# Optimization experiments

Hardware: AMD Instinct MI355X
Metric: run time of the kernel (lower is better)

Reference implementation:

```python
import jax, jax.numpy as jnp
import numpy as np

N_NODES = 100000
N_REL = 8
N_EDGES = 1_600_000
ED = 64   # entity_dim
RD = 64   # relation_dim
H = 4     # attention heads
A = 16    # attention dim per head
D1, D2 = 32, 16  # conv_dim_list


def _leaky(x):
    return jax.nn.leaky_relu(x, 0.01)  # nn.LeakyReLU default slope


def _l2norm(x):
    n = jnp.sqrt(jnp.sum(x * x, axis=1, keepdims=True))
    return x / jnp.maximum(n, 1e-12)  # F.normalize(p=2, dim=1)


def setup_inputs() -> dict:
    key = jax.random.key(0)
    ks = jax.random.split(key, 16)
    s = 0.1
    return dict(
        src=jax.random.randint(ks[0], (N_EDGES,), 0, N_NODES),
        dst=jax.random.randint(ks[1], (N_EDGES,), 0, N_NODES),
        etype=jax.random.randint(ks[2], (N_EDGES,), 0, N_REL),
        node_ids=jnp.arange(N_NODES),
        user_ids=jax.random.randint(ks[3], (1000,), 0, N_NODES),
        item_ids=jax.random.randint(ks[4], (4096,), 0, N_NODES),
        entity_embed=jax.random.normal(ks[5], (N_NODES, ED)) * s,
        rel_embed=jax.random.normal(ks[6], (N_REL, RD)) * s,
        W_R=jax.random.normal(ks[7], (N_REL, ED, RD)) * s,
        W_A=jax.random.normal(ks[8], (RD, H, A)) * s,
        W1_0=jax.random.normal(ks[9], (ED, D1 // H)) * s,
        b1_0=jnp.zeros((D1 // H,)),
        W2_0=jax.random.normal(ks[10], (ED, D1 // H)) * s,
        b2_0=jnp.zeros((D1 // H,)),
        W1_1=jax.random.normal(ks[11], (D1, D2 // H)) * s,
        b1_1=jnp.zeros((D2 // H,)),
        W2_1=jax.random.normal(ks[12], (D1, D2 // H)) * s,
        b2_1=jnp.zeros((D2 // H,)),
    )


def _compute_attention(entity_embed, rel_embed, W_R, W_A, src, dst, etype):
    # relation-specific edge attention: tanh(e_src W_r W_A) * tanh(e_dst W_r W_A + r W_A)
    WA_flat = W_A.reshape(RD, H * A)
    W_ra = jnp.einsum('rij,jk->rik', W_R, WA_flat)          # [R, ED, H*A]
    proj = jnp.einsum('ne,rek->rnk', entity_embed, W_ra)    # [R, N, H*A]
    r_emb_a = rel_embed @ WA_flat                           # [R, H*A]
    r_mul_t = jnp.tanh(proj[etype, src])                    # [E, H*A]
    r_mul_h = jnp.tanh(proj[etype, dst] + r_emb_a[etype])   # [E, H*A]
    att = (r_mul_t * r_mul_h).reshape(-1, H, A).sum(-1)     # [E, H]
    # edge softmax over incoming edges of each dst node, per head
    m = jax.ops.segment_max(att, dst, num_segments=N_NODES)
    m = jnp.where(jnp.isfinite(m), m, 0.0)
    e = jnp.exp(att - m[dst])
    z = jax.ops.segment_sum(e, dst, num_segments=N_NODES)
    return e / jnp.maximum(z[dst], 1e-12)                   # [E, H]


def _bi_layer(ego, att, src, dst, W1, b1, W2, b2, out_dim):
    # u_mul_e + sum: message = node[src] (broadcast over heads) * att[:, :, None]
    in_dim = ego.shape[1]
    msg = ego[src][:, None, :] * att[:, :, None]            # [E, H, in]
    N_h = jax.ops.segment_sum(msg, dst, num_segments=N_NODES)  # [N, H, in]
    node = ego[:, None, :]                                  # [N, 1, in]
    out1 = _leaky((node + N_h).reshape(-1, in_dim) @ W1 + b1).reshape(N_NODES, out_dim)
    out2 = _leaky((node * N_h).reshape(-1, in_dim) @ W2 + b2).reshape(N_NODES, out_dim)
    return out1 + out2  # dropout p=0 (eval)


def reference(src, dst, etype, node_ids, user_ids, item_ids,
              entity_embed, rel_embed, W_R, W_A,
              W1_0, b1_0, W2_0, b2_0, W1_1, b1_1, W2_1, b2_1):
    att = _compute_attention(entity_embed, rel_embed, W_R, W_A, src, dst, etype)
    ego = entity_embed[node_ids]
    ego1 = _bi_layer(ego, att, src, dst, W1_0, b1_0, W2_0, b2_0, D1)
    ego2 = _bi_layer(ego1, att, src, dst, W1_1, b1_1, W2_1, b2_1, D2)
    all_embed = jnp.concatenate([ego, _l2norm(ego1), _l2norm(ego2)], axis=1)  # [N, 112]
    return all_embed[user_ids] @ all_embed[item_ids].T     # [1000, 4096]
```

## Files before the change

### kernel.cpp

```cpp
#include <hip/hip_runtime.h>
#include <hip/hip_bf16.h>
#include <math.h>

#define NN 100000
#define NR 8
#define NE 1600000

typedef __attribute__((ext_vector_type(8))) short short8v;
typedef __attribute__((ext_vector_type(4))) float float4v;
typedef __attribute__((ext_vector_type(2))) float float2v;

__device__ inline float bf2f(unsigned short u) {
  union { unsigned int i; float f; } v; v.i = ((unsigned int)u) << 16; return v.f;
}
__device__ inline unsigned short f2bf(float f) {
  __hip_bfloat16 h = __float2bfloat16(f);
  return *reinterpret_cast<unsigned short*>(&h);
}
__device__ inline float fast_tanh(float x) {
  float ex = __expf(2.f * x);
  return 1.f - 2.f * __builtin_amdgcn_rcpf(ex + 1.f);
}
__device__ inline unsigned char f2fp8(float f) {
  unsigned int p = __builtin_amdgcn_cvt_pk_fp8_f32(f, f, 0, false);
  return (unsigned char)(p & 0xff);
}

__global__ void k_prep(const float* __restrict__ W_R, const float* __restrict__ W_A,
                       const float* __restrict__ rel, unsigned short* __restrict__ Wbf,
                       float* __restrict__ r_emb_a) {
  int tid = blockIdx.x * 256 + threadIdx.x;
  if (tid < NR * 64 * 64) {
    int r = tid >> 12;
    int i = (tid >> 6) & 63;
    int k = tid & 63;
    float acc = 0.f;
    const float* wr = W_R + (r * 64 + i) * 64;
    for (int j = 0; j < 64; ++j) acc += wr[j] * W_A[j * 64 + k];
    Wbf[(r * 64 + k) * 64 + i] = f2bf(acc);
  } else if (tid < NR * 64 * 64 + NR * 64) {
    int idx = tid - NR * 64 * 64;
    int r = idx >> 6, k = idx & 63;
    float acc = 0.f;
    for (int j = 0; j < 64; ++j) acc += rel[r * 64 + j] * W_A[j * 64 + k];
    r_emb_a[idx] = acc;
  }
}

__global__ void k_cvt(const float* __restrict__ E, unsigned short* __restrict__ Ebf) {
  int i = blockIdx.x * 256 + threadIdx.x;
  float4 v = ((const float4*)E)[i];
  ushort4 o;
  o.x = f2bf(v.x); o.y = f2bf(v.y); o.z = f2bf(v.z); o.w = f2bf(v.w);
  ((ushort4*)Ebf)[i] = o;
}

__global__ void k_proj(const unsigned short* __restrict__ Ebf,
                       const unsigned short* __restrict__ Wbf,
                       const float* __restrict__ rea,
                       unsigned char* __restrict__ T1, unsigned char* __restrict__ T2) {
  int wv = threadIdx.x >> 6, lane = threadIdx.x & 63;
  int n0 = blockIdx.x * 64 + wv * 16;
  int mrow = lane & 15, kg = lane >> 4;
  int nodeA = n0 + mrow;
  if (nodeA >= NN) nodeA = NN - 1;
  const short8v a0 = *(const short8v*)(Ebf + (long)nodeA * 64 + kg * 8);
  const short8v a1 = *(const short8v*)(Ebf + (long)nodeA * 64 + 32 + kg * 8);
  int orow = kg * 4;
  for (int ct = 0; ct < 32; ++ct) {
    int c = ct * 16 + mrow;
    const short8v b0 = *(const short8v*)(Wbf + c * 64 + kg * 8);
    const short8v b1 = *(const short8v*)(Wbf + c * 64 + 32 + kg * 8);
    float4v acc = {0.f, 0.f, 0.f, 0.f};
    acc = __builtin_amdgcn_mfma_f32_16x16x32_bf16(a0, b0, acc, 0, 0, 0);
    acc = __builtin_amdgcn_mfma_f32_16x16x32_bf16(a1, b1, acc, 0, 0, 0);
    float rv = rea[c];
    int r = c >> 6, kk = c & 63;
#pragma unroll
    for (int i = 0; i < 4; ++i) {
      int nd = n0 + orow + i;
      if (nd < NN) {
        long base = ((long)r * NN + nd) * 64 + kk;
        T1[base] = f2fp8(fast_tanh(acc[i]));
        T2[base] = f2fp8(fast_tanh(acc[i] + rv));
      }
    }
  }
}

__global__ void k_hist(const int* __restrict__ dst, int* __restrict__ cnt) {
  int e = blockIdx.x * 256 + threadIdx.x;
  if (e < NE) atomicAdd(&cnt[dst[e]], 1);
}

#define SCAN_B 1024
#define NSCAN ((NN + SCAN_B - 1) / SCAN_B)

__global__ void k_scan1(const int* __restrict__ cnt, int* __restrict__ rowp,
                        int* __restrict__ bsum) {
  __shared__ int s[SCAN_B];
  int t = threadIdx.x, g = blockIdx.x * SCAN_B + t;
  s[t] = (g < NN) ? cnt[g] : 0;
  __syncthreads();
  for (int off = 1; off < SCAN_B; off <<= 1) {
    int x = (t >= off) ? s[t - off] : 0;
    __syncthreads();
    s[t] += x;
    __syncthreads();
  }
  if (g < NN) rowp[g + 1] = s[t];
  if (t == SCAN_B - 1) bsum[blockIdx.x] = s[t];
}

__global__ void k_scan2(int* bsum) {
  if (threadIdx.x == 0) {
    int acc = 0;
    for (int i = 0; i < NSCAN; ++i) { int v = bsum[i]; bsum[i] = acc; acc += v; }
  }
}

__global__ void k_scan3(int* rowp, const int* __restrict__ bsum) {
  int t = threadIdx.x, g = blockIdx.x * SCAN_B + t;
  if (g < NN) rowp[g + 1] += bsum[blockIdx.x];
  if (g == 0) rowp[0] = 0;
}

__global__ void k_scatter(const int* __restrict__ src, const int* __restrict__ dst,
                          const int* __restrict__ etype, const int* __restrict__ rowp,
                          int* __restrict__ cur, uint2* __restrict__ rec) {
  int e = blockIdx.x * 256 + threadIdx.x;
  if (e >= NE) return;
  int d = dst[e];
  int p = rowp[d] + atomicAdd(&cur[d], 1);
  uint2 rv;
  rv.x = ((unsigned int)src[e] << 3) | (unsigned int)etype[e];
  rv.y = (unsigned int)d;
  rec[p] = rv;
}

__global__ void k_att(const unsigned char* __restrict__ T1,
                      const unsigned char* __restrict__ T2,
                      const uint2* __restrict__ rec, int* __restrict__ srcs,
                      float* __restrict__ att) {
  int gid = blockIdx.x * 256 + threadIdx.x;
  int e = gid >> 2;
  int h = gid & 3;
  if (e >= NE) return;
  uint2 rv = rec[e];
  int r = rv.x & 7;
  int s = rv.x >> 3;
  int d = (int)rv.y;
  const uint4 av = *(const uint4*)(T1 + ((long)r * NN + s) * 64 + h * 16);
  const uint4 bv = *(const uint4*)(T2 + ((long)r * NN + d) * 64 + h * 16);
  const unsigned int* ap = (const unsigned int*)&av;
  const unsigned int* bp = (const unsigned int*)&bv;
  float acc = 0.f;
#pragma unroll
  for (int i = 0; i < 4; ++i) {
    float2v a0 = __builtin_amdgcn_cvt_pk_f32_fp8(ap[i], false);
    float2v a1 = __builtin_amdgcn_cvt_pk_f32_fp8(ap[i], true);
    float2v b0 = __builtin_amdgcn_cvt_pk_f32_fp8(bp[i], false);
    float2v b1 = __builtin_amdgcn_cvt_pk_f32_fp8(bp[i], true);
    acc += a0.x * b0.x + a0.y * b0.y + a1.x * b1.x + a1.y * b1.y;
  }
  att[gid] = acc;
  if (h == 0) srcs[e] = s;
}

__global__ void k_nodemax(const int* __restrict__ rowp, const float* __restrict__ att,
                          float* __restrict__ minv) {
  int gid = blockIdx.x * 256 + threadIdx.x;
  int n = gid >> 2, h = gid & 3;
  if (n >= NN) return;
  int p0 = rowp[n], p1 = rowp[n + 1];
  float m = -3.4e38f;
  for (int p = p0; p < p1; ++p) m = fmaxf(m, att[p * 4 + h]);
  float z = 0.f;
  for (int p = p0; p < p1; ++p) z += __expf(att[p * 4 + h] - m);
  minv[n * 8 + h] = m;
  minv[n * 8 + 4 + h] = 1.f / fmaxf(z, 1e-12f);
}

__global__ void k_attn(const float* __restrict__ att, const float* __restrict__ minv,
                       const uint2* __restrict__ rec, float* __restrict__ attn) {
  int gid = blockIdx.x * 256 + threadIdx.x;
  int e = gid >> 2, h = gid & 3;
  if (e >= NE) return;
  int d = (int)rec[e].y;
  attn[gid] = __expf(att[gid] - minv[d * 8 + h]) * minv[d * 8 + 4 + h];
}

__global__ void k_fused0(const float* __restrict__ E, const unsigned short* __restrict__ Ebf,
                         const float* __restrict__ attn,
                         const int* __restrict__ rowp, const int* __restrict__ srcs,
                         const float* __restrict__ W1, const float* __restrict__ b1,
                         const float* __restrict__ W2, const float* __restrict__ b2,
                         float* __restrict__ ego1, unsigned short* __restrict__ ego1bf) {
  __shared__ float wt1[8][68], wt2[8][68];
  __shared__ float bb[16];
  __shared__ float s1[4][4][68], s2[4][4][68];
  int t = threadIdx.x;
  for (int i = t; i < 512; i += 256) {
    int d = i >> 3, j = i & 7;
    wt1[j][d] = W1[i];
    wt2[j][d] = W2[i];
  }
  if (t < 8) bb[t] = b1[t];
  else if (t < 16) bb[t] = b2[t - 8];
  __syncthreads();
  int wv = t >> 6, lane = t & 63;
  int n = blockIdx.x * 4 + wv;
  int p0 = rowp[n], p1 = rowp[n + 1];
  int g = lane >> 4, q = lane & 15;
  float acc[4][4];
#pragma unroll
  for (int h = 0; h < 4; ++h)
#pragma unroll
    for (int j = 0; j < 4; ++j) acc[h][j] = 0.f;
  for (int p = p0 + g; p < p1; p += 4) {
    int s = srcs[p];
    float4 a = ((const float4*)attn)[p];
    ushort4 ev = *(const ushort4*)(Ebf + s * 64 + q * 4);
    float e0 = bf2f(ev.x), e1 = bf2f(ev.y), e2 = bf2f(ev.z), e3 = bf2f(ev.w);
    acc[0][0] += a.x * e0; acc[0][1] += a.x * e1; acc[0][2] += a.x * e2; acc[0][3] += a.x * e3;
    acc[1][0] += a.y * e0; acc[1][1] += a.y * e1; acc[1][2] += a.y * e2; acc[1][3] += a.y * e3;
    acc[2][0] += a.z * e0; acc[2][1] += a.z * e1; acc[2][2] += a.z * e2; acc[2][3] += a.z * e3;
    acc[3][0] += a.w * e0; acc[3][1] += a.w * e1; acc[3][2] += a.w * e2; acc[3][3] += a.w * e3;
  }
#pragma unroll
  for (int h = 0; h < 4; ++h)
#pragma unroll
    for (int j = 0; j < 4; ++j) {
      acc[h][j] += __shfl_xor(acc[h][j], 16);
      acc[h][j] += __shfl_xor(acc[h][j], 32);
    }
  if (lane < 16) {
    float4 edv = *(const float4*)(E + n * 64 + q * 4);
#pragma unroll
    for (int h = 0; h < 4; ++h) {
      float4 v1, v2;
      v1.x = edv.x + acc[h][0]; v2.x = edv.x * acc[h][0];
      v1.y = edv.y + acc[h][1]; v2.y = edv.y * acc[h][1];
      v1.z = edv.z + acc[h][2]; v2.z = edv.z * acc[h][2];
      v1.w = edv.w + acc[h][3]; v2.w = edv.w * acc[h][3];
      *(float4*)&s1[wv][h][q * 4] = v1;
      *(float4*)&s2[wv][h][q * 4] = v2;
    }
  }
  __syncthreads();
  int h = (lane >> 3) & 3, j = lane & 7;
  const float* sp = (lane < 32) ? &s1[wv][h][0] : &s2[wv][h][0];
  const float* wp = (lane < 32) ? &wt1[j][0] : &wt2[j][0];
  float o = 0.f;
#pragma unroll
  for (int d = 0; d < 64; d += 4) {
    float4 sv = *(const float4*)(sp + d);
    float4 wv4 = *(const float4*)(wp + d);
    o += sv.x * wv4.x + sv.y * wv4.y + sv.z * wv4.z + sv.w * wv4.w;
  }
  o += (lane < 32) ? bb[j] : bb[8 + j];
  o = (o >= 0.f) ? o : 0.01f * o;
  float other = __shfl_xor(o, 32);
  if (lane < 32) {
    float r = o + other;
    ego1[n * 32 + h * 8 + j] = r;
    ego1bf[n * 32 + h * 8 + j] = f2bf(r);
  }
}

__global__ void k_fused1(const float* __restrict__ ego1, const unsigned short* __restrict__ E1bf,
                         const float* __restrict__ attn,
                         const int* __restrict__ rowp, const int* __restrict__ srcs,
                         const float* __restrict__ W1, const float* __restrict__ b1,
                         const float* __restrict__ W2, const float* __restrict__ b2,
                         float* __restrict__ ego2) {
  __shared__ float wt1[4][36], wt2[4][36], bb[8];
  __shared__ float s1[4][4][36], s2[4][4][36];
  int t = threadIdx.x;
  if (t < 128) { int d = t >> 2, j = t & 3; wt1[j][d] = W1[t]; wt2[j][d] = W2[t]; }
  if (t < 4) bb[t] = b1[t];
  else if (t < 8) bb[t] = b2[t - 4];
  __syncthreads();
  int wv = t >> 6, lane = t & 63;
  int n = blockIdx.x * 4 + wv;
  int p0 = rowp[n], p1 = rowp[n + 1];
  int g = lane >> 3, q = lane & 7;
  float acc[4][4];
#pragma unroll
  for (int h = 0; h < 4; ++h)
#pragma unroll
    for (int j = 0; j < 4; ++j) acc[h][j] = 0.f;
  for (int p = p0 + g; p < p1; p += 8) {
    int s = srcs[p];
    float4 a = ((const float4*)attn)[p];
    ushort4 ev = *(const ushort4*)(E1bf + s * 32 + q * 4);
    float e0 = bf2f(ev.x), e1 = bf2f(ev.y), e2 = bf2f(ev.z), e3 = bf2f(ev.w);
    acc[0][0] += a.x * e0; acc[0][1] += a.x * e1; acc[0][2] += a.x * e2; acc[0][3] += a.x * e3;
    acc[1][0] += a.y * e0; acc[1][1] += a.y * e1; acc[1][2] += a.y * e2; acc[1][3] += a.y * e3;
    acc[2][0] += a.z * e0; acc[2][1] += a.z * e1; acc[2][2] += a.z * e2; acc[2][3] += a.z * e3;
    acc[3][0] += a.w * e0; acc[3][1] += a.w * e1; acc[3][2] += a.w * e2; acc[3][3] += a.w * e3;
  }
#pragma unroll
  for (int h = 0; h < 4; ++h)
#pragma unroll
    for (int j = 0; j < 4; ++j) {
      acc[h][j] += __shfl_xor(acc[h][j], 8);
      acc[h][j] += __shfl_xor(acc[h][j], 16);
      acc[h][j] += __shfl_xor(acc[h][j], 32);
    }
  if (lane < 8) {
    float4 e1v = *(const float4*)(ego1 + n * 32 + q * 4);
#pragma unroll
    for (int h = 0; h < 4; ++h) {
      float4 v1, v2;
      v1.x = e1v.x + acc[h][0]; v2.x = e1v.x * acc[h][0];
      v1.y = e1v.y + acc[h][1]; v2.y = e1v.y * acc[h][1];
      v1.z = e1v.z + acc[h][2]; v2.z = e1v.z * acc[h][2];
      v1.w = e1v.w + acc[h][3]; v2.w = e1v.w * acc[h][3];
      *(float4*)&s1[wv][h][q * 4] = v1;
      *(float4*)&s2[wv][h][q * 4] = v2;
    }
  }
  __syncthreads();
  if (lane < 32) {
    int h = (lane >> 2) & 3, j = lane & 3;
    const float* sp = (lane < 16) ? &s1[wv][h][0] : &s2[wv][h][0];
    const float* wp = (lane < 16) ? &wt1[j][0] : &wt2[j][0];
    float o = 0.f;
#pragma unroll
    for (int d = 0; d < 32; d += 4) {
      float4 sv = *(const float4*)(sp + d);
      float4 wv4 = *(const float4*)(wp + d);
      o += sv.x * wv4.x + sv.y * wv4.y + sv.z * wv4.z + sv.w * wv4.w;
    }
    o += (lane < 16) ? bb[j] : bb[4 + j];
    o = (o >= 0.f) ? o : 0.01f * o;
    float other = __shfl_xor(o, 16);
    if (lane < 16) ego2[n * 16 + h * 4 + j] = o + other;
  }
}

__global__ void k_uv(const float* __restrict__ E, const float* __restrict__ E1,
                     const float* __restrict__ E2, const int* __restrict__ uid,
                     const int* __restrict__ iid, float* __restrict__ U,
                     float* __restrict__ V) {
  int row = (blockIdx.x * 256 + threadIdx.x) >> 6;
  int lane = threadIdx.x & 63;
  if (row >= 1000 + 4096) return;
  int id = (row < 1000) ? uid[row] : iid[row - 1000];
  float* dest = (row < 1000) ? (U + row * 112) : (V + (row - 1000) * 112);
  float v1 = (lane < 32) ? E1[id * 32 + lane] : 0.f;
  float s1 = v1 * v1;
  for (int m = 1; m < 64; m <<= 1) s1 += __shfl_xor(s1, m);
  float v2 = (lane < 16) ? E2[id * 16 + lane] : 0.f;
  float s2 = v2 * v2;
  for (int m = 1; m < 64; m <<= 1) s2 += __shfl_xor(s2, m);
  float i1 = 1.f / fmaxf(sqrtf(s1), 1e-12f);
  float i2 = 1.f / fmaxf(sqrtf(s2), 1e-12f);
  dest[lane] = E[id * 64 + lane];
  if (lane < 32) dest[64 + lane] = v1 * i1;
  if (lane < 16) dest[96 + lane] = v2 * i2;
}

__global__ void k_gemm(const float* __restrict__ U, const float* __restrict__ V,
                       float* __restrict__ C) {
  __shared__ float Us[16][113], Vs[16][113];
  int tx = threadIdx.x & 15, ty = threadIdx.x >> 4;
  int u0 = blockIdx.y * 16, v0 = blockIdx.x * 16;
  for (int i = threadIdx.x; i < 16 * 112; i += 256) {
    int rr = i / 112, cc = i % 112;
    int ur = u0 + rr;
    Us[rr][cc] = (ur < 1000) ? U[ur * 112 + cc] : 0.f;
    Vs[rr][cc] = V[(v0 + rr) * 112 + cc];
  }
  __syncthreads();
  int u = u0 + ty;
  if (u >= 1000) return;
  float acc = 0.f;
#pragma unroll
  for (int k = 0; k < 112; ++k) acc += Us[ty][k] * Vs[tx][k];
  C[u * 4096 + v0 + tx] = acc;
}

extern "C" void kernel_launch(void* const* d_in, const int* in_sizes, int n_in,
                              void* d_out, int out_size, void* d_ws, size_t ws_size,
                              hipStream_t stream) {
  const int* src = (const int*)d_in[0];
  const int* dst = (const int*)d_in[1];
  const int* etype = (const int*)d_in[2];
  const int* uid = (const int*)d_in[4];
  const int* iid = (const int*)d_in[5];
  const float* entity = (const float*)d_in[6];
  const float* rel = (const float*)d_in[7];
  const float* W_R = (const float*)d_in[8];
  const float* W_A = (const float*)d_in[9];
  const float* W1_0 = (const float*)d_in[10];
  const float* b1_0 = (const float*)d_in[11];
  const float* W2_0 = (const float*)d_in[12];
  const float* b2_0 = (const float*)d_in[13];
  const float* W1_1 = (const float*)d_in[14];
  const float* b1_1 = (const float*)d_in[15];
  const float* W2_1 = (const float*)d_in[16];
  const float* b2_1 = (const float*)d_in[17];
  float* out = (float*)d_out;

  char* ws = (char*)d_ws;
  unsigned char*  T1   = (unsigned char*) (ws + 0);
  float*          ego1 = (float*)         (ws + 0);
  unsigned short* e1bf = (unsigned short*)(ws + 12800000);
  float*          ego2 = (float*)         (ws + 19200000);
  float*          U    = (float*)         (ws + 25600000);
  float*          V    = (float*)         (ws + 26048000);
  unsigned char*  T2   = (unsigned char*) (ws + 51200000);
  float*          attn = (float*)         (ws + 51200000);
  float*          att  = (float*)         (ws + 102400000);
  uint2*          rec  = (uint2*)         (ws + 128000000);
  int*            srcs = (int*)           (ws + 140800000);
  int*            rowp = (int*)           (ws + 147200000);
  int*            cnt  = (int*)           (ws + 147600128);
  int*            bsum = (int*)           (ws + 148000256);
  unsigned short* Wbf  = (unsigned short*)(ws + 148000768);
  float*          rea  = (float*)         (ws + 148066304);
  unsigned short* Ebf  = (unsigned short*)(ws + 148068352);
  float*          minv = (float*)         (ws + 160868352);

  hipMemsetAsync(cnt, 0, NN * sizeof(int), stream);
  k_prep<<<130, 256, 0, stream>>>(W_R, W_A, rel, Wbf, rea);
  k_cvt<<<6250, 256, 0, stream>>>(entity, Ebf);
  k_proj<<<(NN + 63) / 64, 256, 0, stream>>>(Ebf, Wbf, rea, T1, T2);
  k_hist<<<NE / 256, 256, 0, stream>>>(dst, cnt);
  k_scan1<<<NSCAN, SCAN_B, 0, stream>>>(cnt, rowp, bsum);
  k_scan2<<<1, 64, 0, stream>>>(bsum);
  k_scan3<<<NSCAN, SCAN_B, 0, stream>>>(rowp, bsum);
  hipMemsetAsync(cnt, 0, NN * sizeof(int), stream);
  k_scatter<<<NE / 256, 256, 0, stream>>>(src, dst, etype, rowp, cnt, rec);
  k_att<<<NE * 4 / 256, 256, 0, stream>>>(T1, T2, rec, srcs, att);
  k_nodemax<<<(NN * 4 + 255) / 256, 256, 0, stream>>>(rowp, att, minv);
  k_attn<<<NE * 4 / 256, 256, 0, stream>>>(att, minv, rec, attn);
  k_fused0<<<NN / 4, 256, 0, stream>>>(entity, Ebf, attn, rowp, srcs,
                                       W1_0, b1_0, W2_0, b2_0, ego1, e1bf);
  k_fused1<<<NN / 4, 256, 0, stream>>>(ego1, e1bf, attn, rowp, srcs,
                                       W1_1, b1_1, W2_1, b2_1, ego2);
  k_uv<<<(1000 + 4096 + 3) / 4, 256, 0, stream>>>(entity, ego1, ego2, uid, iid, U, V);
  k_gemm<<<dim3(4096 / 16, (1000 + 15) / 16), 256, 0, stream>>>(U, V, out);
}
```

Before: 615.0 us.

## Store projections node-major with packed fp8 writes and fuse softmax normalization into aggregation

The projection kernel swaps MFMA operands so each lane holds four consecutive channels of one node. It packs them into one 32-bit fp8 word and stores into a node-major [N][R*64] layout. Before, it wrote single bytes scattered across relation-major planes. The edge attention gather now reads from this node-major layout. The separate edge-softmax normalization kernel is removed, and both aggregation layers recompute exp(att - max) * inv_sum inline, which saves an E*4 float write and read pass but repeats the exp in two kernels.

```diff
diff --git a/kernel.cpp b/kernel.cpp
--- a/kernel.cpp
+++ b/kernel.cpp
@@ -20,10 +20,6 @@
 __device__ inline float fast_tanh(float x) {
   float ex = __expf(2.f * x);
   return 1.f - 2.f * __builtin_amdgcn_rcpf(ex + 1.f);
-}
-__device__ inline unsigned char f2fp8(float f) {
-  unsigned int p = __builtin_amdgcn_cvt_pk_fp8_f32(f, f, 0, false);
-  return (unsigned char)(p & 0xff);
 }
 
 __global__ void k_prep(const float* __restrict__ W_R, const float* __restrict__ W_A,
@@ -58,32 +54,31 @@
 __global__ void k_proj(const unsigned short* __restrict__ Ebf,
                        const unsigned short* __restrict__ Wbf,
                        const float* __restrict__ rea,
-                       unsigned char* __restrict__ T1, unsigned char* __restrict__ T2) {
+                       unsigned char* __restrict__ T1n, unsigned char* __restrict__ T2n) {
   int wv = threadIdx.x >> 6, lane = threadIdx.x & 63;
   int n0 = blockIdx.x * 64 + wv * 16;
   int mrow = lane & 15, kg = lane >> 4;
-  int nodeA = n0 + mrow;
-  if (nodeA >= NN) nodeA = NN - 1;
-  const short8v a0 = *(const short8v*)(Ebf + (long)nodeA * 64 + kg * 8);
-  const short8v a1 = *(const short8v*)(Ebf + (long)nodeA * 64 + 32 + kg * 8);
-  int orow = kg * 4;
+  int node = n0 + mrow;
+  int nodeC = (node < NN) ? node : NN - 1;
+  bool ok = (node < NN);
+  const short8v b0 = *(const short8v*)(Ebf + (long)nodeC * 64 + kg * 8);
+  const short8v b1 = *(const short8v*)(Ebf + (long)nodeC * 64 + 32 + kg * 8);
   for (int ct = 0; ct < 32; ++ct) {
-    int c = ct * 16 + mrow;
-    const short8v b0 = *(const short8v*)(Wbf + c * 64 + kg * 8);
-    const short8v b1 = *(const short8v*)(Wbf + c * 64 + 32 + kg * 8);
+    int ca = ct * 16 + mrow;
+    const short8v a0 = *(const short8v*)(Wbf + ca * 64 + kg * 8);
+    const short8v a1 = *(const short8v*)(Wbf + ca * 64 + 32 + kg * 8);
     float4v acc = {0.f, 0.f, 0.f, 0.f};
     acc = __builtin_amdgcn_mfma_f32_16x16x32_bf16(a0, b0, acc, 0, 0, 0);
     acc = __builtin_amdgcn_mfma_f32_16x16x32_bf16(a1, b1, acc, 0, 0, 0);
-    float rv = rea[c];
-    int r = c >> 6, kk = c & 63;
-#pragma unroll
-    for (int i = 0; i < 4; ++i) {
-      int nd = n0 + orow + i;
-      if (nd < NN) {
-        long base = ((long)r * NN + nd) * 64 + kk;
-        T1[base] = f2fp8(fast_tanh(acc[i]));
-        T2[base] = f2fp8(fast_tanh(acc[i] + rv));
-      }
+    int c0 = ct * 16 + kg * 4;
+    float4 rv4 = *(const float4*)(rea + c0);
+    unsigned int p1 = __builtin_amdgcn_cvt_pk_fp8_f32(fast_tanh(acc[0]), fast_tanh(acc[1]), 0u, false);
+    p1 = __builtin_amdgcn_cvt_pk_fp8_f32(fast_tanh(acc[2]), fast_tanh(acc[3]), p1, true);
+    unsigned int p2 = __builtin_amdgcn_cvt_pk_fp8_f32(fast_tanh(acc[0] + rv4.x), fast_tanh(acc[1] + rv4.y), 0u, false);
+    p2 = __builtin_amdgcn_cvt_pk_fp8_f32(fast_tanh(acc[2] + rv4.z), fast_tanh(acc[3] + rv4.w), p2, true);
+    if (ok) {
+      *(unsigned int*)(T1n + (long)node * 512 + c0) = p1;
+      *(unsigned int*)(T2n + (long)node * 512 + c0) = p2;
     }
   }
 }
@@ -138,8 +133,8 @@
   rec[p] = rv;
 }
 
-__global__ void k_att(const unsigned char* __restrict__ T1,
-                      const unsigned char* __restrict__ T2,
+__global__ void k_att(const unsigned char* __restrict__ T1n,
+                      const unsigned char* __restrict__ T2n,
                       const uint2* __restrict__ rec, int* __restrict__ srcs,
                       float* __restrict__ att) {
   int gid = blockIdx.x * 256 + threadIdx.x;
@@ -150,8 +145,8 @@
   int r = rv.x & 7;
   int s = rv.x >> 3;
   int d = (int)rv.y;
-  const uint4 av = *(const uint4*)(T1 + ((long)r * NN + s) * 64 + h * 16);
-  const uint4 bv = *(const uint4*)(T2 + ((long)r * NN + d) * 64 + h * 16);
+  const uint4 av = *(const uint4*)(T1n + (long)s * 512 + r * 64 + h * 16);
+  const uint4 bv = *(const uint4*)(T2n + (long)d * 512 + r * 64 + h * 16);
   const unsigned int* ap = (const unsigned int*)&av;
   const unsigned int* bp = (const unsigned int*)&bv;
   float acc = 0.f;
@@ -181,17 +176,8 @@
   minv[n * 8 + 4 + h] = 1.f / fmaxf(z, 1e-12f);
 }
 
-__global__ void k_attn(const float* __restrict__ att, const float* __restrict__ minv,
-                       const uint2* __restrict__ rec, float* __restrict__ attn) {
-  int gid = blockIdx.x * 256 + threadIdx.x;
-  int e = gid >> 2, h = gid & 3;
-  if (e >= NE) return;
-  int d = (int)rec[e].y;
-  attn[gid] = __expf(att[gid] - minv[d * 8 + h]) * minv[d * 8 + 4 + h];
-}
-
 __global__ void k_fused0(const float* __restrict__ E, const unsigned short* __restrict__ Ebf,
-                         const float* __restrict__ attn,
+                         const float* __restrict__ att, const float* __restrict__ minv,
                          const int* __restrict__ rowp, const int* __restrict__ srcs,
                          const float* __restrict__ W1, const float* __restrict__ b1,
                          const float* __restrict__ W2, const float* __restrict__ b2,
@@ -212,6 +198,8 @@
   int n = blockIdx.x * 4 + wv;
   int p0 = rowp[n], p1 = rowp[n + 1];
   int g = lane >> 4, q = lane & 15;
+  float4 mh = *(const float4*)(minv + n * 8);
+  float4 zh = *(const float4*)(minv + n * 8 + 4);
   float acc[4][4];
 #pragma unroll
   for (int h = 0; h < 4; ++h)
@@ -219,7 +207,11 @@
     for (int j = 0; j < 4; ++j) acc[h][j] = 0.f;
   for (int p = p0 + g; p < p1; p += 4) {
     int s = srcs[p];
-    float4 a = ((const float4*)attn)[p];
+    float4 a = ((const float4*)att)[p];
+    a.x = __expf(a.x - mh.x) * zh.x;
+    a.y = __expf(a.y - mh.y) * zh.y;
+    a.z = __expf(a.z - mh.z) * zh.z;
+    a.w = __expf(a.w - mh.w) * zh.w;
     ushort4 ev = *(const ushort4*)(Ebf + s * 64 + q * 4);
     float e0 = bf2f(ev.x), e1 = bf2f(ev.y), e2 = bf2f(ev.z), e3 = bf2f(ev.w);
     acc[0][0] += a.x * e0; acc[0][1] += a.x * e1; acc[0][2] += a.x * e2; acc[0][3] += a.x * e3;
@@ -269,7 +261,7 @@
 }
 
 __global__ void k_fused1(const float* __restrict__ ego1, const unsigned short* __restrict__ E1bf,
-                         const float* __restrict__ attn,
+                         const float* __restrict__ att, const float* __restrict__ minv,
                          const int* __restrict__ rowp, const int* __restrict__ srcs,
                          const float* __restrict__ W1, const float* __restrict__ b1,
                          const float* __restrict__ W2, const float* __restrict__ b2,
@@ -285,6 +277,8 @@
   int n = blockIdx.x * 4 + wv;
   int p0 = rowp[n], p1 = rowp[n + 1];
   int g = lane >> 3, q = lane & 7;
+  float4 mh = *(const float4*)(minv + n * 8);
+  float4 zh = *(const float4*)(minv + n * 8 + 4);
   float acc[4][4];
 #pragma unroll
   for (int h = 0; h < 4; ++h)
@@ -292,7 +286,11 @@
     for (int j = 0; j < 4; ++j) acc[h][j] = 0.f;
   for (int p = p0 + g; p < p1; p += 8) {
     int s = srcs[p];
-    float4 a = ((const float4*)attn)[p];
+    float4 a = ((const float4*)att)[p];
+    a.x = __expf(a.x - mh.x) * zh.x;
+    a.y = __expf(a.y - mh.y) * zh.y;
+    a.z = __expf(a.z - mh.z) * zh.z;
+    a.w = __expf(a.w - mh.w) * zh.w;
     ushort4 ev = *(const ushort4*)(E1bf + s * 32 + q * 4);
     float e0 = bf2f(ev.x), e1 = bf2f(ev.y), e2 = bf2f(ev.z), e3 = bf2f(ev.w);
     acc[0][0] += a.x * e0; acc[0][1] += a.x * e1; acc[0][2] += a.x * e2; acc[0][3] += a.x * e3;
@@ -405,14 +403,13 @@
   float* out = (float*)d_out;
 
   char* ws = (char*)d_ws;
-  unsigned char*  T1   = (unsigned char*) (ws + 0);
+  unsigned char*  T1n  = (unsigned char*) (ws + 0);
   float*          ego1 = (float*)         (ws + 0);
   unsigned short* e1bf = (unsigned short*)(ws + 12800000);
   float*          ego2 = (float*)         (ws + 19200000);
   float*          U    = (float*)         (ws + 25600000);
   float*          V    = (float*)         (ws + 26048000);
-  unsigned char*  T2   = (unsigned char*) (ws + 51200000);
-  float*          attn = (float*)         (ws + 51200000);
+  unsigned char*  T2n  = (unsigned char*) (ws + 51200000);
   float*          att  = (float*)         (ws + 102400000);
   uint2*          rec  = (uint2*)         (ws + 128000000);
   int*            srcs = (int*)           (ws + 140800000);
@@ -427,19 +424,18 @@
   hipMemsetAsync(cnt, 0, NN * sizeof(int), stream);
   k_prep<<<130, 256, 0, stream>>>(W_R, W_A, rel, Wbf, rea);
   k_cvt<<<6250, 256, 0, stream>>>(entity, Ebf);
-  k_proj<<<(NN + 63) / 64, 256, 0, stream>>>(Ebf, Wbf, rea, T1, T2);
+  k_proj<<<(NN + 63) / 64, 256, 0, stream>>>(Ebf, Wbf, rea, T1n, T2n);
   k_hist<<<NE / 256, 256, 0, stream>>>(dst, cnt);
   k_scan1<<<NSCAN, SCAN_B, 0, stream>>>(cnt, rowp, bsum);
   k_scan2<<<1, 64, 0, stream>>>(bsum);
   k_scan3<<<NSCAN, SCAN_B, 0, stream>>>(rowp, bsum);
   hipMemsetAsync(cnt, 0, NN * sizeof(int), stream);
   k_scatter<<<NE / 256, 256, 0, stream>>>(src, dst, etype, rowp, cnt, rec);
-  k_att<<<NE * 4 / 256, 256, 0, stream>>>(T1, T2, rec, srcs, att);
+  k_att<<<NE * 4 / 256, 256, 0, stream>>>(T1n, T2n, rec, srcs, att);
   k_nodemax<<<(NN * 4 + 255) / 256, 256, 0, stream>>>(rowp, att, minv);
-  k_attn<<<NE * 4 / 256, 256, 0, stream>>>(att, minv, rec, attn);
-  k_fused0<<<NN / 4, 256, 0, stream>>>(entity, Ebf, attn, rowp, srcs,
+  k_fused0<<<NN / 4, 256, 0, stream>>>(entity, Ebf, att, minv, rowp, srcs,
                                        W1_0, b1_0, W2_0, b2_0, ego1, e1bf);
-  k_fused1<<<NN / 4, 256, 0, stream>>>(ego1, e1bf, attn, rowp, srcs,
+  k_fused1<<<NN / 4, 256, 0, stream>>>(ego1, e1bf, att, minv, rowp, srcs,
                                        W1_1, b1_1, W2_1, b2_1, ego2);
   k_uv<<<(1000 + 4096 + 3) / 4, 256, 0, stream>>>(entity, ego1, ego2, uid, iid, U, V);
   k_gemm<<<dim3(4096 / 16, (1000 + 15) / 16), 256, 0, stream>>>(U, V, out);
```

After: 594.8 us. 3.3% less time.
